# Kernel tuning notes

Measured on AMD Instinct MI355X. Metric: run time of the kernel, lower is better.

## Reference

```python
import jax, jax.numpy as jnp
import numpy as np

N = 50000
E = 600000
F_IN = 128
F_OUT = 128


def setup_inputs() -> dict:
    key = jax.random.key(0)
    k = jax.random.split(key, 8)
    x = jax.random.normal(k[0], (N, F_IN), dtype=jnp.float32)
    edge_index = jax.random.randint(k[1], (2, E), 0, N, dtype=jnp.int64)
    edge_weight = jax.random.uniform(k[2], (E,), dtype=jnp.float32)
    # glorot-initialized linear params (w1 is dead code in the original, kept for faithfulness)
    s = float(np.sqrt(6.0 / (F_IN + F_OUT)))
    W1 = jax.random.uniform(k[3], (F_IN, F_OUT), minval=-s, maxval=s, dtype=jnp.float32)
    b1 = jnp.zeros((F_OUT,), dtype=jnp.float32)
    W2 = jax.random.uniform(k[4], (F_IN, F_OUT), minval=-s, maxval=s, dtype=jnp.float32)
    b2 = jnp.zeros((F_OUT,), dtype=jnp.float32)
    a = jnp.full((1,), 0.5, dtype=jnp.float32)
    b = jnp.full((1,), 0.5, dtype=jnp.float32)
    return {"x": x, "edge_index": edge_index, "edge_weight": edge_weight,
            "W1": W1, "b1": b1, "W2": W2, "b2": b2, "a": a, "b": b}


def reference(x, edge_index, edge_weight, W1, b1, W2, b2, a, b):
    # wh_1 = self.w1(x)  (computed but unused in the original forward)
    wh_1 = x @ W1 + b1  # noqa: F841 (dead, DCE'd under jit)
    src, dst = edge_index[0], edge_index[1]
    # gather neighbor features [E, F_IN], scatter-sum to destination nodes [N, F_IN]
    x_j = jax.ops.segment_sum(x[src], dst, num_segments=N)
    wh_2 = x_j @ W2 + b2
    return wh_2
```

## Files before the change

kernel.cpp:

```cpp
#include <hip/hip_runtime.h>

#define F 128
#define CAP 64
#define TR 64
#define KC 32
#define LDA 36
#define LDW 160

__global__ __launch_bounds__(256) void init_kernel(
    const int* __restrict__ ei, const float* __restrict__ x,
    int* __restrict__ flag, int* __restrict__ zero_arr,
    unsigned int* __restrict__ xh, int N, int M)
{
    int i = blockIdx.x * 256 + threadIdx.x;
    if (i < M) {
        float2 v = reinterpret_cast<const float2*>(x)[i];
        unsigned ux = __float_as_uint(v.x);
        unsigned uy = __float_as_uint(v.y);
        unsigned lo = (ux + 0x7fffu + ((ux >> 16) & 1u)) >> 16;
        unsigned hi = (uy + 0x7fffu + ((uy >> 16) & 1u)) >> 16;
        xh[i] = lo | (hi << 16);
    }
    if (i < N) zero_arr[i] = 0;
    if (i == 0) {
        int or_hi = ei[1] | ei[3] | ei[5] | ei[7] | ei[9] | ei[11] | ei[13] | ei[15];
        *flag = (or_hi == 0) ? 1 : 0;
    }
}

__device__ __forceinline__ void load_edge(const int* __restrict__ ei, int is64,
                                          int E, int e, int& s, int& d)
{
    if (is64) {
        s = reinterpret_cast<const int2*>(ei)[e].x;
        d = reinterpret_cast<const int2*>(ei)[(size_t)E + e].x;
    } else {
        s = ei[e];
        d = ei[E + e];
    }
}

__global__ __launch_bounds__(256) void position_bucket_kernel(
    const int* __restrict__ ei, const int* __restrict__ flag_p,
    int* __restrict__ cursor, int* __restrict__ csr_src, int E)
{
    int e = blockIdx.x * 256 + threadIdx.x;
    if (e >= E) return;
    int s, d;
    load_edge(ei, *flag_p, E, e, s, d);
    int slot = atomicAdd(&cursor[d], 1);
    if (slot < CAP) csr_src[d * CAP + slot] = s;
}

__device__ __forceinline__ float4 bf16x4_to_f4(uint2 u)
{
    float4 f;
    f.x = __uint_as_float(u.x << 16);
    f.y = __uint_as_float(u.x & 0xffff0000u);
    f.z = __uint_as_float(u.y << 16);
    f.w = __uint_as_float(u.y & 0xffff0000u);
    return f;
}

__global__ __launch_bounds__(256) void gather_bucket_bf16_kernel(
    const unsigned int* __restrict__ xh, const int* __restrict__ ei,
    const int* __restrict__ flag_p, const int* __restrict__ cursor,
    const int* __restrict__ csr_src, float* __restrict__ agg, int N, int E)
{
    int node = blockIdx.x * 4 + (threadIdx.x >> 6);
    if (node >= N) return;
    int lane = threadIdx.x & 63;
    int half = lane >> 5;
    int col = lane & 31;
    int deg = cursor[node];

    const uint2* x2 = reinterpret_cast<const uint2*>(xh);
    float4 a0 = make_float4(0.f, 0.f, 0.f, 0.f);
    float4 a1 = make_float4(0.f, 0.f, 0.f, 0.f);

    if (deg <= CAP) {
        int sv = (lane < deg) ? csr_src[node * CAP + lane] : 0;
        int i = 0;
        for (; i + 3 < deg; i += 4) {
            int e0 = __shfl(sv, i + half);
            int e1 = __shfl(sv, i + 2 + half);
            float4 v0 = bf16x4_to_f4(x2[(size_t)e0 * 32 + col]);
            float4 v1 = bf16x4_to_f4(x2[(size_t)e1 * 32 + col]);
            a0.x += v0.x; a0.y += v0.y; a0.z += v0.z; a0.w += v0.w;
            a1.x += v1.x; a1.y += v1.y; a1.z += v1.z; a1.w += v1.w;
        }
        for (; i + 1 < deg; i += 2) {
            int e0 = __shfl(sv, i + half);
            float4 v0 = bf16x4_to_f4(x2[(size_t)e0 * 32 + col]);
            a0.x += v0.x; a0.y += v0.y; a0.z += v0.z; a0.w += v0.w;
        }
        if (i < deg) {
            int e0 = __shfl(sv, i);
            if (half == 0) {
                float4 v = bf16x4_to_f4(x2[(size_t)e0 * 32 + col]);
                a0.x += v.x; a0.y += v.y; a0.z += v.z; a0.w += v.w;
            }
        }
    } else {
        int is64 = *flag_p;
        for (int base = 0; base < E; base += 64) {
            int e = base + lane;
            int s = 0, d = -1;
            if (e < E) load_edge(ei, is64, E, e, s, d);
            unsigned long long m = __ballot(d == node);
            while (m) {
                int i = __ffsll((long long)m) - 1;
                m &= m - 1;
                int sb = __shfl(s, i);
                float4 v = bf16x4_to_f4(x2[(size_t)sb * 32 + col]);
                if (half == 0) { a0.x += v.x; a0.y += v.y; a0.z += v.z; a0.w += v.w; }
            }
        }
    }
    a0.x += a1.x; a0.y += a1.y; a0.z += a1.z; a0.w += a1.w;
    a0.x += __shfl_xor(a0.x, 32);
    a0.y += __shfl_xor(a0.y, 32);
    a0.z += __shfl_xor(a0.z, 32);
    a0.w += __shfl_xor(a0.w, 32);
    if (half == 0)
        reinterpret_cast<float4*>(agg)[(size_t)node * 32 + col] = a0;
}

__global__ __launch_bounds__(256) void hist_kernel(
    const int* __restrict__ ei, const int* __restrict__ flag_p,
    int* __restrict__ counts, int E)
{
    int e = blockIdx.x * 256 + threadIdx.x;
    if (e >= E) return;
    int s, d;
    load_edge(ei, *flag_p, E, e, s, d);
    atomicAdd(&counts[d], 1);
}

__global__ __launch_bounds__(256) void scan1_kernel(
    const int* __restrict__ counts, int* __restrict__ locoff,
    int* __restrict__ cursor, int* __restrict__ blocksums, int N)
{
    __shared__ int sh[256];
    int t = threadIdx.x;
    int i = blockIdx.x * 256 + t;
    int v = (i < N) ? counts[i] : 0;
    sh[t] = v;
    __syncthreads();
    int inc = v;
    #pragma unroll
    for (int ofs = 1; ofs < 256; ofs <<= 1) {
        int add = (t >= ofs) ? sh[t - ofs] : 0;
        __syncthreads();
        inc += add;
        sh[t] = inc;
        __syncthreads();
    }
    if (i < N) { locoff[i] = inc - v; cursor[i] = inc - v; }
    if (t == 255) blocksums[blockIdx.x] = inc;
}

__global__ __launch_bounds__(256) void scan2_kernel(
    int* __restrict__ blocksums, int* __restrict__ blockoffs, int nblk)
{
    __shared__ int sh[256];
    int t = threadIdx.x;
    int v = (t < nblk) ? blocksums[t] : 0;
    sh[t] = v;
    __syncthreads();
    int inc = v;
    #pragma unroll
    for (int ofs = 1; ofs < 256; ofs <<= 1) {
        int add = (t >= ofs) ? sh[t - ofs] : 0;
        __syncthreads();
        inc += add;
        sh[t] = inc;
        __syncthreads();
    }
    if (t < nblk) blockoffs[t] = inc - v;
}

__global__ __launch_bounds__(256) void position_kernel(
    const int* __restrict__ ei, const int* __restrict__ flag_p,
    int* __restrict__ cursor, const int* __restrict__ blockoffs,
    int* __restrict__ csr_src, int E)
{
    int e = blockIdx.x * 256 + threadIdx.x;
    if (e >= E) return;
    int s, d;
    load_edge(ei, *flag_p, E, e, s, d);
    int pos = atomicAdd(&cursor[d], 1) + blockoffs[d >> 8];
    csr_src[pos] = s;
}

__global__ __launch_bounds__(256) void gather_csr_bf16_kernel(
    const unsigned int* __restrict__ xh, const int* __restrict__ locoff,
    const int* __restrict__ blockoffs, const int* __restrict__ counts,
    const int* __restrict__ csr_src, float* __restrict__ agg, int N)
{
    int node = blockIdx.x * 4 + (threadIdx.x >> 6);
    if (node >= N) return;
    int lane = threadIdx.x & 63;
    int half = lane >> 5;
    int col = lane & 31;
    int start = locoff[node] + blockoffs[node >> 8];
    int deg = counts[node];

    const uint2* x2 = reinterpret_cast<const uint2*>(xh);
    float4 a0 = make_float4(0.f, 0.f, 0.f, 0.f);
    float4 a1 = make_float4(0.f, 0.f, 0.f, 0.f);

    for (int base = 0; base < deg; base += 64) {
        int rem = deg - base; if (rem > 64) rem = 64;
        int sv = (lane < rem) ? csr_src[start + base + lane] : 0;
        int i = 0;
        for (; i + 3 < rem; i += 4) {
            int e0 = __shfl(sv, i + half);
            int e1 = __shfl(sv, i + 2 + half);
            float4 v0 = bf16x4_to_f4(x2[(size_t)e0 * 32 + col]);
            float4 v1 = bf16x4_to_f4(x2[(size_t)e1 * 32 + col]);
            a0.x += v0.x; a0.y += v0.y; a0.z += v0.z; a0.w += v0.w;
            a1.x += v1.x; a1.y += v1.y; a1.z += v1.z; a1.w += v1.w;
        }
        for (; i + 1 < rem; i += 2) {
            int e0 = __shfl(sv, i + half);
            float4 v0 = bf16x4_to_f4(x2[(size_t)e0 * 32 + col]);
            a0.x += v0.x; a0.y += v0.y; a0.z += v0.z; a0.w += v0.w;
        }
        if (i < rem) {
            int e0 = __shfl(sv, i);
            if (half == 0) {
                float4 v = bf16x4_to_f4(x2[(size_t)e0 * 32 + col]);
                a0.x += v.x; a0.y += v.y; a0.z += v.z; a0.w += v.w;
            }
        }
    }
    a0.x += a1.x; a0.y += a1.y; a0.z += a1.z; a0.w += a1.w;
    a0.x += __shfl_xor(a0.x, 32);
    a0.y += __shfl_xor(a0.y, 32);
    a0.z += __shfl_xor(a0.z, 32);
    a0.w += __shfl_xor(a0.w, 32);
    if (half == 0)
        reinterpret_cast<float4*>(agg)[(size_t)node * 32 + col] = a0;
}

__global__ __launch_bounds__(256) void gather_csr_f32_kernel(
    const float* __restrict__ x, const int* __restrict__ locoff,
    const int* __restrict__ blockoffs, const int* __restrict__ counts,
    const int* __restrict__ csr_src, float* __restrict__ agg, int N)
{
    int node = blockIdx.x * 4 + (threadIdx.x >> 6);
    if (node >= N) return;
    int lane = threadIdx.x & 63;
    int half = lane >> 5;
    int col = lane & 31;
    int start = locoff[node] + blockoffs[node >> 8];
    int deg = counts[node];

    const float4* x4 = reinterpret_cast<const float4*>(x);
    float4 a0 = make_float4(0.f, 0.f, 0.f, 0.f);
    float4 a1 = make_float4(0.f, 0.f, 0.f, 0.f);

    for (int base = 0; base < deg; base += 64) {
        int rem = deg - base; if (rem > 64) rem = 64;
        int sv = (lane < rem) ? csr_src[start + base + lane] : 0;
        int i = 0;
        for (; i + 3 < rem; i += 4) {
            int e0 = __shfl(sv, i + half);
            int e1 = __shfl(sv, i + 2 + half);
            float4 v0 = x4[(size_t)e0 * 32 + col];
            float4 v1 = x4[(size_t)e1 * 32 + col];
            a0.x += v0.x; a0.y += v0.y; a0.z += v0.z; a0.w += v0.w;
            a1.x += v1.x; a1.y += v1.y; a1.z += v1.z; a1.w += v1.w;
        }
        for (; i + 1 < rem; i += 2) {
            int e0 = __shfl(sv, i + half);
            float4 v0 = x4[(size_t)e0 * 32 + col];
            a0.x += v0.x; a0.y += v0.y; a0.z += v0.z; a0.w += v0.w;
        }
        if (i < rem) {
            int e0 = __shfl(sv, i);
            if (half == 0) {
                float4 v = x4[(size_t)e0 * 32 + col];
                a0.x += v.x; a0.y += v.y; a0.z += v.z; a0.w += v.w;
            }
        }
    }
    a0.x += a1.x; a0.y += a1.y; a0.z += a1.z; a0.w += a1.w;
    a0.x += __shfl_xor(a0.x, 32);
    a0.y += __shfl_xor(a0.y, 32);
    a0.z += __shfl_xor(a0.z, 32);
    a0.w += __shfl_xor(a0.w, 32);
    if (half == 0)
        reinterpret_cast<float4*>(agg)[(size_t)node * 32 + col] = a0;
}

__global__ __launch_bounds__(256) void scatter_kernel(
    const float* __restrict__ x, const int* __restrict__ ei,
    const int* __restrict__ flag_p, float* __restrict__ agg, int E)
{
    int tid = blockIdx.x * 256 + threadIdx.x;
    int e = tid >> 5;
    if (e >= E) return;
    int c = (tid & 31) << 2;
    int s, d;
    load_edge(ei, *flag_p, E, e, s, d);
    float4 v = *reinterpret_cast<const float4*>(x + (size_t)s * F + c);
    float* o = agg + (size_t)d * F + c;
    unsafeAtomicAdd(o + 0, v.x);
    unsafeAtomicAdd(o + 1, v.y);
    unsafeAtomicAdd(o + 2, v.z);
    unsafeAtomicAdd(o + 3, v.w);
}

__global__ __launch_bounds__(256) void gemm_kernel(
    float* __restrict__ io, const float* __restrict__ W,
    const float* __restrict__ bias, int N)
{
    __shared__ float sA[TR * LDA];
    __shared__ float sW[KC * LDW];
    const int t = threadIdx.x;
    const int row0 = blockIdx.x * TR;
    const int g = t & 7;
    const int r = t >> 3;

    float acc[2][16];
    #pragma unroll
    for (int i = 0; i < 2; ++i)
        #pragma unroll
        for (int j = 0; j < 16; ++j) acc[i][j] = 0.0f;

    for (int kc = 0; kc < F; kc += KC) {
        #pragma unroll
        for (int u = 0; u < 2; ++u) {
            int idx = u * 256 + t;
            int row = idx >> 3;
            int k4 = (idx & 7) * 4;
            int grow = row0 + row;
            float4 v = (grow < N)
                ? *reinterpret_cast<const float4*>(io + (size_t)grow * F + kc + k4)
                : make_float4(0.f, 0.f, 0.f, 0.f);
            *reinterpret_cast<float4*>(&sA[row * LDA + k4]) = v;
        }
        #pragma unroll
        for (int u = 0; u < 4; ++u) {
            int idx = u * 256 + t;
            int kk = idx >> 5;
            int f4 = (idx & 31) * 4;
            float4 v = *reinterpret_cast<const float4*>(W + (size_t)(kc + kk) * F + f4);
            int chunk = f4 >> 4;
            int within = f4 & 15;
            *reinterpret_cast<float4*>(&sW[kk * LDW + chunk * 20 + within]) = v;
        }
        __syncthreads();

        #pragma unroll 8
        for (int kk = 0; kk < KC; ++kk) {
            const float* wp = &sW[kk * LDW + g * 20];
            const float4 w0 = *reinterpret_cast<const float4*>(wp + 0);
            const float4 w1 = *reinterpret_cast<const float4*>(wp + 4);
            const float4 w2 = *reinterpret_cast<const float4*>(wp + 8);
            const float4 w3 = *reinterpret_cast<const float4*>(wp + 12);
            #pragma unroll
            for (int i = 0; i < 2; ++i) {
                const float xv = sA[(r * 2 + i) * LDA + kk];
                acc[i][0]  += xv * w0.x;  acc[i][1]  += xv * w0.y;
                acc[i][2]  += xv * w0.z;  acc[i][3]  += xv * w0.w;
                acc[i][4]  += xv * w1.x;  acc[i][5]  += xv * w1.y;
                acc[i][6]  += xv * w1.z;  acc[i][7]  += xv * w1.w;
                acc[i][8]  += xv * w2.x;  acc[i][9]  += xv * w2.y;
                acc[i][10] += xv * w2.z;  acc[i][11] += xv * w2.w;
                acc[i][12] += xv * w3.x;  acc[i][13] += xv * w3.y;
                acc[i][14] += xv * w3.z;  acc[i][15] += xv * w3.w;
            }
        }
        __syncthreads();
    }

    float bv[16];
    #pragma unroll
    for (int j = 0; j < 16; ++j) bv[j] = bias[g * 16 + j];
    #pragma unroll
    for (int i = 0; i < 2; ++i) {
        int row = row0 + r * 2 + i;
        if (row < N) {
            float* o = io + (size_t)row * F + g * 16;
            #pragma unroll
            for (int j4 = 0; j4 < 4; ++j4) {
                float4 v;
                v.x = acc[i][j4 * 4 + 0] + bv[j4 * 4 + 0];
                v.y = acc[i][j4 * 4 + 1] + bv[j4 * 4 + 1];
                v.z = acc[i][j4 * 4 + 2] + bv[j4 * 4 + 2];
                v.w = acc[i][j4 * 4 + 3] + bv[j4 * 4 + 3];
                *reinterpret_cast<float4*>(o + j4 * 4) = v;
            }
        }
    }
}

extern "C" void kernel_launch(void* const* d_in, const int* in_sizes, int n_in,
                              void* d_out, int out_size, void* d_ws, size_t ws_size,
                              hipStream_t stream) {
    const float* x  = (const float*)d_in[0];
    const int*   ei = (const int*)d_in[1];
    const float* W2 = (const float*)d_in[5];
    const float* b2 = (const float*)d_in[6];
    float* out = (float*)d_out;

    const int N = in_sizes[0] / F;
    const int E = in_sizes[2];
    const int nblk = (N + 255) / 256;
    const int M = N * (F / 2);
    const int eblk = (E + 255) / 256;

    int* ws = (int*)d_ws;
    size_t needA = (size_t)(16 + N + N * CAP + M) * sizeof(int);
    size_t needC = (size_t)(16 + 3 * N + 2 * nblk + E) * sizeof(int);
    size_t needB = needC + (size_t)M * sizeof(int);

    if (ws_size >= needA) {
        int* flag    = ws;
        int* cursor  = flag + 16;
        int* csr_src = cursor + N;
        unsigned int* xh = (unsigned int*)(csr_src + (size_t)N * CAP);

        int iblk = ((M > N ? M : N) + 255) / 256;
        init_kernel<<<iblk, 256, 0, stream>>>(ei, x, flag, cursor, xh, N, M);
        position_bucket_kernel<<<eblk, 256, 0, stream>>>(ei, flag, cursor, csr_src, E);
        gather_bucket_bf16_kernel<<<(N + 3) / 4, 256, 0, stream>>>(
            xh, ei, flag, cursor, csr_src, out, N, E);
    } else if (ws_size >= needC) {
        int* flag      = ws;
        int* counts    = flag + 16;
        int* locoff    = counts + N;
        int* cursor    = locoff + N;
        int* blocksums = cursor + N;
        int* blockoffs = blocksums + nblk;
        int* csr_src   = blockoffs + nblk;
        unsigned int* xh = (unsigned int*)(csr_src + E);
        int do_bf16 = (ws_size >= needB) ? 1 : 0;
        int Mx = do_bf16 ? M : 0;

        int iblk = (((Mx > N ? Mx : N)) + 255) / 256;
        init_kernel<<<iblk, 256, 0, stream>>>(ei, x, flag, counts, xh, N, Mx);
        hist_kernel<<<eblk, 256, 0, stream>>>(ei, flag, counts, E);
        scan1_kernel<<<nblk, 256, 0, stream>>>(counts, locoff, cursor, blocksums, N);
        scan2_kernel<<<1, 256, 0, stream>>>(blocksums, blockoffs, nblk);
        position_kernel<<<eblk, 256, 0, stream>>>(ei, flag, cursor, blockoffs, csr_src, E);
        if (do_bf16)
            gather_csr_bf16_kernel<<<(N + 3) / 4, 256, 0, stream>>>(
                xh, locoff, blockoffs, counts, csr_src, out, N);
        else
            gather_csr_f32_kernel<<<(N + 3) / 4, 256, 0, stream>>>(
                x, locoff, blockoffs, counts, csr_src, out, N);
    } else {
        int* flag = ws;
        init_kernel<<<1, 64, 0, stream>>>(ei, x, flag, flag + 16, nullptr, 0, 0);
        hipMemsetAsync(out, 0, (size_t)N * F * sizeof(float), stream);
        scatter_kernel<<<(E * 32 + 255) / 256, 256, 0, stream>>>(x, ei, flag, out, E);
    }

    gemm_kernel<<<(N + TR - 1) / TR, 256, 0, stream>>>(out, W2, b2, N);
}
```

Baseline: 187.3 us.

## Fuse gather with GEMM and merge bf16 conversion into edge bucketing

The main path now fuses neighbour aggregation with the dense W2 projection. Each block gathers 64 rows into shared memory and multiplies them by W2 directly, so the aggregated matrix is no longer written to and re-read from global memory. The bf16 conversion of x is folded into the edge positioning kernel, which also loads two edges per thread with vector loads. A small zero kernel replaces the old init. The risk is lower gather parallelism, since each wave handles 16 rows in sequence and fewer blocks are launched. The large shared-memory footprint of about 54 KB may also limit occupancy.

```diff
diff --git a/kernel.cpp b/kernel.cpp
--- a/kernel.cpp
+++ b/kernel.cpp
@@ -2,10 +2,230 @@
 
 #define F 128
 #define CAP 64
+#define KC 32
+#define LDAF 132
+#define LDW 160
 #define TR 64
-#define KC 32
 #define LDA 36
-#define LDW 160
+
+__global__ __launch_bounds__(256) void zero_kernel(
+    const int* __restrict__ ei, int* __restrict__ flag,
+    int* __restrict__ cursor, int N)
+{
+    int i = blockIdx.x * 256 + threadIdx.x;
+    if (i < N) cursor[i] = 0;
+    if (i == 0) {
+        int or_hi = ei[1] | ei[3] | ei[5] | ei[7] | ei[9] | ei[11] | ei[13] | ei[15];
+        *flag = (or_hi == 0) ? 1 : 0;
+    }
+}
+
+__device__ __forceinline__ void load_edge(const int* __restrict__ ei, int is64,
+                                          int E, int e, int& s, int& d)
+{
+    if (is64) {
+        s = reinterpret_cast<const int2*>(ei)[e].x;
+        d = reinterpret_cast<const int2*>(ei)[(size_t)E + e].x;
+    } else {
+        s = ei[e];
+        d = ei[E + e];
+    }
+}
+
+__global__ __launch_bounds__(256) void posconv_kernel(
+    const int* __restrict__ ei, const float* __restrict__ x,
+    const int* __restrict__ flag_p, int* __restrict__ cursor,
+    int* __restrict__ csr_src, unsigned int* __restrict__ xh,
+    int E, int M)
+{
+    const int tid = blockIdx.x * 256 + threadIdx.x;
+    const int T = gridDim.x * 256;
+    const int is64 = *flag_p;
+
+    int e0 = 2 * tid;
+    if (e0 < E) {
+        if (e0 + 1 < E) {
+            int s0, d0, s1, d1;
+            if (is64) {
+                int4 sv = reinterpret_cast<const int4*>(ei)[tid];
+                int4 dv = reinterpret_cast<const int4*>(ei)[(size_t)(E >> 1) + tid];
+                s0 = sv.x; s1 = sv.z; d0 = dv.x; d1 = dv.z;
+            } else {
+                int2 sv = reinterpret_cast<const int2*>(ei)[tid];
+                int2 dv = reinterpret_cast<const int2*>(ei)[(size_t)(E >> 1) + tid];
+                s0 = sv.x; s1 = sv.y; d0 = dv.x; d1 = dv.y;
+            }
+            int slot0 = atomicAdd(&cursor[d0], 1);
+            int slot1 = atomicAdd(&cursor[d1], 1);
+            if (slot0 < CAP) csr_src[d0 * CAP + slot0] = s0;
+            if (slot1 < CAP) csr_src[d1 * CAP + slot1] = s1;
+        } else {
+            int s, d;
+            load_edge(ei, is64, E, e0, s, d);
+            int slot = atomicAdd(&cursor[d], 1);
+            if (slot < CAP) csr_src[d * CAP + slot] = s;
+        }
+    }
+
+    const float2* x2 = reinterpret_cast<const float2*>(x);
+    for (int j = tid; j < M; j += T) {
+        float2 v = x2[j];
+        unsigned ux = __float_as_uint(v.x);
+        unsigned uy = __float_as_uint(v.y);
+        unsigned lo = (ux + 0x7fffu + ((ux >> 16) & 1u)) >> 16;
+        unsigned hi = (uy + 0x7fffu + ((uy >> 16) & 1u)) >> 16;
+        xh[j] = lo | (hi << 16);
+    }
+}
+
+__device__ __forceinline__ float4 bf16x4_to_f4(uint2 u)
+{
+    float4 f;
+    f.x = __uint_as_float(u.x << 16);
+    f.y = __uint_as_float(u.x & 0xffff0000u);
+    f.z = __uint_as_float(u.y << 16);
+    f.w = __uint_as_float(u.y & 0xffff0000u);
+    return f;
+}
+
+__global__ __launch_bounds__(256) void gather_gemm_kernel(
+    const unsigned int* __restrict__ xh, const int* __restrict__ ei,
+    const int* __restrict__ flag_p, const int* __restrict__ cursor,
+    const int* __restrict__ csr_src, const float* __restrict__ W,
+    const float* __restrict__ bias, float* __restrict__ out, int N, int E)
+{
+    __shared__ float sA[64 * LDAF];
+    __shared__ float sW[KC * LDW];
+    const int t = threadIdx.x;
+    const int row0 = blockIdx.x * 64;
+    const int w = t >> 6;
+    const int lane = t & 63;
+    const int half = lane >> 5;
+    const int col = lane & 31;
+
+    const uint2* x2 = reinterpret_cast<const uint2*>(xh);
+
+    for (int j = 0; j < 16; ++j) {
+        int lrow = w * 16 + j;
+        int node = row0 + lrow;
+        float4 a0 = make_float4(0.f, 0.f, 0.f, 0.f);
+        float4 a1 = make_float4(0.f, 0.f, 0.f, 0.f);
+        if (node < N) {
+            int deg = cursor[node];
+            if (deg <= CAP) {
+                int sv = (lane < deg) ? csr_src[node * CAP + lane] : 0;
+                int i = 0;
+                for (; i + 3 < deg; i += 4) {
+                    int e0 = __shfl(sv, i + half);
+                    int e1 = __shfl(sv, i + 2 + half);
+                    float4 v0 = bf16x4_to_f4(x2[(size_t)e0 * 32 + col]);
+                    float4 v1 = bf16x4_to_f4(x2[(size_t)e1 * 32 + col]);
+                    a0.x += v0.x; a0.y += v0.y; a0.z += v0.z; a0.w += v0.w;
+                    a1.x += v1.x; a1.y += v1.y; a1.z += v1.z; a1.w += v1.w;
+                }
+                for (; i + 1 < deg; i += 2) {
+                    int e0 = __shfl(sv, i + half);
+                    float4 v0 = bf16x4_to_f4(x2[(size_t)e0 * 32 + col]);
+                    a0.x += v0.x; a0.y += v0.y; a0.z += v0.z; a0.w += v0.w;
+                }
+                if (i < deg) {
+                    int e0 = __shfl(sv, i);
+                    if (half == 0) {
+                        float4 v = bf16x4_to_f4(x2[(size_t)e0 * 32 + col]);
+                        a0.x += v.x; a0.y += v.y; a0.z += v.z; a0.w += v.w;
+                    }
+                }
+            } else {
+                int is64 = *flag_p;
+                for (int base = 0; base < E; base += 64) {
+                    int e = base + lane;
+                    int s = 0, d = -1;
+                    if (e < E) load_edge(ei, is64, E, e, s, d);
+                    unsigned long long m = __ballot(d == node);
+                    while (m) {
+                        int i = __ffsll((long long)m) - 1;
+                        m &= m - 1;
+                        int sb = __shfl(s, i);
+                        float4 v = bf16x4_to_f4(x2[(size_t)sb * 32 + col]);
+                        if (half == 0) { a0.x += v.x; a0.y += v.y; a0.z += v.z; a0.w += v.w; }
+                    }
+                }
+            }
+        }
+        a0.x += a1.x; a0.y += a1.y; a0.z += a1.z; a0.w += a1.w;
+        a0.x += __shfl_xor(a0.x, 32);
+        a0.y += __shfl_xor(a0.y, 32);
+        a0.z += __shfl_xor(a0.z, 32);
+        a0.w += __shfl_xor(a0.w, 32);
+        if (half == 0)
+            *reinterpret_cast<float4*>(&sA[lrow * LDAF + col * 4]) = a0;
+    }
+    __syncthreads();
+
+    const int g = t & 7;
+    const int r = t >> 3;
+    float acc[2][16];
+    #pragma unroll
+    for (int i = 0; i < 2; ++i)
+        #pragma unroll
+        for (int j = 0; j < 16; ++j) acc[i][j] = 0.0f;
+
+    for (int kc = 0; kc < F; kc += KC) {
+        #pragma unroll
+        for (int u = 0; u < 4; ++u) {
+            int idx = u * 256 + t;
+            int kk = idx >> 5;
+            int f4 = (idx & 31) * 4;
+            float4 v = *reinterpret_cast<const float4*>(W + (size_t)(kc + kk) * F + f4);
+            int chunk = f4 >> 4;
+            int within = f4 & 15;
+            *reinterpret_cast<float4*>(&sW[kk * LDW + chunk * 20 + within]) = v;
+        }
+        __syncthreads();
+
+        #pragma unroll 8
+        for (int kk = 0; kk < KC; ++kk) {
+            const float* wp = &sW[kk * LDW + g * 20];
+            const float4 w0 = *reinterpret_cast<const float4*>(wp + 0);
+            const float4 w1 = *reinterpret_cast<const float4*>(wp + 4);
+            const float4 w2 = *reinterpret_cast<const float4*>(wp + 8);
+            const float4 w3 = *reinterpret_cast<const float4*>(wp + 12);
+            #pragma unroll
+            for (int i = 0; i < 2; ++i) {
+                const float xv = sA[(r * 2 + i) * LDAF + kc + kk];
+                acc[i][0]  += xv * w0.x;  acc[i][1]  += xv * w0.y;
+                acc[i][2]  += xv * w0.z;  acc[i][3]  += xv * w0.w;
+                acc[i][4]  += xv * w1.x;  acc[i][5]  += xv * w1.y;
+                acc[i][6]  += xv * w1.z;  acc[i][7]  += xv * w1.w;
+                acc[i][8]  += xv * w2.x;  acc[i][9]  += xv * w2.y;
+                acc[i][10] += xv * w2.z;  acc[i][11] += xv * w2.w;
+                acc[i][12] += xv * w3.x;  acc[i][13] += xv * w3.y;
+                acc[i][14] += xv * w3.z;  acc[i][15] += xv * w3.w;
+            }
+        }
+        __syncthreads();
+    }
+
+    float bv[16];
+    #pragma unroll
+    for (int j = 0; j < 16; ++j) bv[j] = bias[g * 16 + j];
+    #pragma unroll
+    for (int i = 0; i < 2; ++i) {
+        int row = row0 + r * 2 + i;
+        if (row < N) {
+            float* o = out + (size_t)row * F + g * 16;
+            #pragma unroll
+            for (int j4 = 0; j4 < 4; ++j4) {
+                float4 v;
+                v.x = acc[i][j4 * 4 + 0] + bv[j4 * 4 + 0];
+                v.y = acc[i][j4 * 4 + 1] + bv[j4 * 4 + 1];
+                v.z = acc[i][j4 * 4 + 2] + bv[j4 * 4 + 2];
+                v.w = acc[i][j4 * 4 + 3] + bv[j4 * 4 + 3];
+                *reinterpret_cast<float4*>(o + j4 * 4) = v;
+            }
+        }
+    }
+}
 
 __global__ __launch_bounds__(256) void init_kernel(
     const int* __restrict__ ei, const float* __restrict__ x,
@@ -28,18 +248,6 @@
     }
 }
 
-__device__ __forceinline__ void load_edge(const int* __restrict__ ei, int is64,
-                                          int E, int e, int& s, int& d)
-{
-    if (is64) {
-        s = reinterpret_cast<const int2*>(ei)[e].x;
-        d = reinterpret_cast<const int2*>(ei)[(size_t)E + e].x;
-    } else {
-        s = ei[e];
-        d = ei[E + e];
-    }
-}
-
 __global__ __launch_bounds__(256) void position_bucket_kernel(
     const int* __restrict__ ei, const int* __restrict__ flag_p,
     int* __restrict__ cursor, int* __restrict__ csr_src, int E)
@@ -52,18 +260,8 @@
     if (slot < CAP) csr_src[d * CAP + slot] = s;
 }
 
-__device__ __forceinline__ float4 bf16x4_to_f4(uint2 u)
-{
-    float4 f;
-    f.x = __uint_as_float(u.x << 16);
-    f.y = __uint_as_float(u.x & 0xffff0000u);
-    f.z = __uint_as_float(u.y << 16);
-    f.w = __uint_as_float(u.y & 0xffff0000u);
-    return f;
-}
-
-__global__ __launch_bounds__(256) void gather_bucket_bf16_kernel(
-    const unsigned int* __restrict__ xh, const int* __restrict__ ei,
+__global__ __launch_bounds__(256) void gather_bucket_f32_kernel(
+    const float* __restrict__ x, const int* __restrict__ ei,
     const int* __restrict__ flag_p, const int* __restrict__ cursor,
     const int* __restrict__ csr_src, float* __restrict__ agg, int N, int E)
 {
@@ -74,7 +272,7 @@
     int col = lane & 31;
     int deg = cursor[node];
 
-    const uint2* x2 = reinterpret_cast<const uint2*>(xh);
+    const float4* x4 = reinterpret_cast<const float4*>(x);
     float4 a0 = make_float4(0.f, 0.f, 0.f, 0.f);
     float4 a1 = make_float4(0.f, 0.f, 0.f, 0.f);
 
@@ -84,20 +282,20 @@
         for (; i + 3 < deg; i += 4) {
             int e0 = __shfl(sv, i + half);
             int e1 = __shfl(sv, i + 2 + half);
-            float4 v0 = bf16x4_to_f4(x2[(size_t)e0 * 32 + col]);
-            float4 v1 = bf16x4_to_f4(x2[(size_t)e1 * 32 + col]);
+            float4 v0 = x4[(size_t)e0 * 32 + col];
+            float4 v1 = x4[(size_t)e1 * 32 + col];
             a0.x += v0.x; a0.y += v0.y; a0.z += v0.z; a0.w += v0.w;
             a1.x += v1.x; a1.y += v1.y; a1.z += v1.z; a1.w += v1.w;
         }
         for (; i + 1 < deg; i += 2) {
             int e0 = __shfl(sv, i + half);
-            float4 v0 = bf16x4_to_f4(x2[(size_t)e0 * 32 + col]);
+            float4 v0 = x4[(size_t)e0 * 32 + col];
             a0.x += v0.x; a0.y += v0.y; a0.z += v0.z; a0.w += v0.w;
         }
         if (i < deg) {
             int e0 = __shfl(sv, i);
             if (half == 0) {
-                float4 v = bf16x4_to_f4(x2[(size_t)e0 * 32 + col]);
+                float4 v = x4[(size_t)e0 * 32 + col];
                 a0.x += v.x; a0.y += v.y; a0.z += v.z; a0.w += v.w;
             }
         }
@@ -112,177 +310,8 @@
                 int i = __ffsll((long long)m) - 1;
                 m &= m - 1;
                 int sb = __shfl(s, i);
-                float4 v = bf16x4_to_f4(x2[(size_t)sb * 32 + col]);
+                float4 v = x4[(size_t)sb * 32 + col];
                 if (half == 0) { a0.x += v.x; a0.y += v.y; a0.z += v.z; a0.w += v.w; }
-            }
-        }
-    }
-    a0.x += a1.x; a0.y += a1.y; a0.z += a1.z; a0.w += a1.w;
-    a0.x += __shfl_xor(a0.x, 32);
-    a0.y += __shfl_xor(a0.y, 32);
-    a0.z += __shfl_xor(a0.z, 32);
-    a0.w += __shfl_xor(a0.w, 32);
-    if (half == 0)
-        reinterpret_cast<float4*>(agg)[(size_t)node * 32 + col] = a0;
-}
-
-__global__ __launch_bounds__(256) void hist_kernel(
-    const int* __restrict__ ei, const int* __restrict__ flag_p,
-    int* __restrict__ counts, int E)
-{
-    int e = blockIdx.x * 256 + threadIdx.x;
-    if (e >= E) return;
-    int s, d;
-    load_edge(ei, *flag_p, E, e, s, d);
-    atomicAdd(&counts[d], 1);
-}
-
-__global__ __launch_bounds__(256) void scan1_kernel(
-    const int* __restrict__ counts, int* __restrict__ locoff,
-    int* __restrict__ cursor, int* __restrict__ blocksums, int N)
-{
-    __shared__ int sh[256];
-    int t = threadIdx.x;
-    int i = blockIdx.x * 256 + t;
-    int v = (i < N) ? counts[i] : 0;
-    sh[t] = v;
-    __syncthreads();
-    int inc = v;
-    #pragma unroll
-    for (int ofs = 1; ofs < 256; ofs <<= 1) {
-        int add = (t >= ofs) ? sh[t - ofs] : 0;
-        __syncthreads();
-        inc += add;
-        sh[t] = inc;
-        __syncthreads();
-    }
-    if (i < N) { locoff[i] = inc - v; cursor[i] = inc - v; }
-    if (t == 255) blocksums[blockIdx.x] = inc;
-}
-
-__global__ __launch_bounds__(256) void scan2_kernel(
-    int* __restrict__ blocksums, int* __restrict__ blockoffs, int nblk)
-{
-    __shared__ int sh[256];
-    int t = threadIdx.x;
-    int v = (t < nblk) ? blocksums[t] : 0;
-    sh[t] = v;
-    __syncthreads();
-    int inc = v;
-    #pragma unroll
-    for (int ofs = 1; ofs < 256; ofs <<= 1) {
-        int add = (t >= ofs) ? sh[t - ofs] : 0;
-        __syncthreads();
-        inc += add;
-        sh[t] = inc;
-        __syncthreads();
-    }
-    if (t < nblk) blockoffs[t] = inc - v;
-}
-
-__global__ __launch_bounds__(256) void position_kernel(
-    const int* __restrict__ ei, const int* __restrict__ flag_p,
-    int* __restrict__ cursor, const int* __restrict__ blockoffs,
-    int* __restrict__ csr_src, int E)
-{
-    int e = blockIdx.x * 256 + threadIdx.x;
-    if (e >= E) return;
-    int s, d;
-    load_edge(ei, *flag_p, E, e, s, d);
-    int pos = atomicAdd(&cursor[d], 1) + blockoffs[d >> 8];
-    csr_src[pos] = s;
-}
-
-__global__ __launch_bounds__(256) void gather_csr_bf16_kernel(
-    const unsigned int* __restrict__ xh, const int* __restrict__ locoff,
-    const int* __restrict__ blockoffs, const int* __restrict__ counts,
-    const int* __restrict__ csr_src, float* __restrict__ agg, int N)
-{
-    int node = blockIdx.x * 4 + (threadIdx.x >> 6);
-    if (node >= N) return;
-    int lane = threadIdx.x & 63;
-    int half = lane >> 5;
-    int col = lane & 31;
-    int start = locoff[node] + blockoffs[node >> 8];
-    int deg = counts[node];
-
-    const uint2* x2 = reinterpret_cast<const uint2*>(xh);
-    float4 a0 = make_float4(0.f, 0.f, 0.f, 0.f);
-    float4 a1 = make_float4(0.f, 0.f, 0.f, 0.f);
-
-    for (int base = 0; base < deg; base += 64) {
-        int rem = deg - base; if (rem > 64) rem = 64;
-        int sv = (lane < rem) ? csr_src[start + base + lane] : 0;
-        int i = 0;
-        for (; i + 3 < rem; i += 4) {
-            int e0 = __shfl(sv, i + half);
-            int e1 = __shfl(sv, i + 2 + half);
-            float4 v0 = bf16x4_to_f4(x2[(size_t)e0 * 32 + col]);
-            float4 v1 = bf16x4_to_f4(x2[(size_t)e1 * 32 + col]);
-            a0.x += v0.x; a0.y += v0.y; a0.z += v0.z; a0.w += v0.w;
-            a1.x += v1.x; a1.y += v1.y; a1.z += v1.z; a1.w += v1.w;
-        }
-        for (; i + 1 < rem; i += 2) {
-            int e0 = __shfl(sv, i + half);
-            float4 v0 = bf16x4_to_f4(x2[(size_t)e0 * 32 + col]);
-            a0.x += v0.x; a0.y += v0.y; a0.z += v0.z; a0.w += v0.w;
-        }
-        if (i < rem) {
-            int e0 = __shfl(sv, i);
-            if (half == 0) {
-                float4 v = bf16x4_to_f4(x2[(size_t)e0 * 32 + col]);
-                a0.x += v.x; a0.y += v.y; a0.z += v.z; a0.w += v.w;
-            }
-        }
-    }
-    a0.x += a1.x; a0.y += a1.y; a0.z += a1.z; a0.w += a1.w;
-    a0.x += __shfl_xor(a0.x, 32);
-    a0.y += __shfl_xor(a0.y, 32);
-    a0.z += __shfl_xor(a0.z, 32);
-    a0.w += __shfl_xor(a0.w, 32);
-    if (half == 0)
-        reinterpret_cast<float4*>(agg)[(size_t)node * 32 + col] = a0;
-}
-
-__global__ __launch_bounds__(256) void gather_csr_f32_kernel(
-    const float* __restrict__ x, const int* __restrict__ locoff,
-    const int* __restrict__ blockoffs, const int* __restrict__ counts,
-    const int* __restrict__ csr_src, float* __restrict__ agg, int N)
-{
-    int node = blockIdx.x * 4 + (threadIdx.x >> 6);
-    if (node >= N) return;
-    int lane = threadIdx.x & 63;
-    int half = lane >> 5;
-    int col = lane & 31;
-    int start = locoff[node] + blockoffs[node >> 8];
-    int deg = counts[node];
-
-    const float4* x4 = reinterpret_cast<const float4*>(x);
-    float4 a0 = make_float4(0.f, 0.f, 0.f, 0.f);
-    float4 a1 = make_float4(0.f, 0.f, 0.f, 0.f);
-
-    for (int base = 0; base < deg; base += 64) {
-        int rem = deg - base; if (rem > 64) rem = 64;
-        int sv = (lane < rem) ? csr_src[start + base + lane] : 0;
-        int i = 0;
-        for (; i + 3 < rem; i += 4) {
-            int e0 = __shfl(sv, i + half);
-            int e1 = __shfl(sv, i + 2 + half);
-            float4 v0 = x4[(size_t)e0 * 32 + col];
-            float4 v1 = x4[(size_t)e1 * 32 + col];
-            a0.x += v0.x; a0.y += v0.y; a0.z += v0.z; a0.w += v0.w;
-            a1.x += v1.x; a1.y += v1.y; a1.z += v1.z; a1.w += v1.w;
-        }
-        for (; i + 1 < rem; i += 2) {
-            int e0 = __shfl(sv, i + half);
-            float4 v0 = x4[(size_t)e0 * 32 + col];
-            a0.x += v0.x; a0.y += v0.y; a0.z += v0.z; a0.w += v0.w;
-        }
-        if (i < rem) {
-            int e0 = __shfl(sv, i);
-            if (half == 0) {
-                float4 v = x4[(size_t)e0 * 32 + col];
-                a0.x += v.x; a0.y += v.y; a0.z += v.z; a0.w += v.w;
             }
         }
     }
@@ -414,9 +443,8 @@
     const int eblk = (E + 255) / 256;
 
     int* ws = (int*)d_ws;
-    size_t needA = (size_t)(16 + N + N * CAP + M) * sizeof(int);
-    size_t needC = (size_t)(16 + 3 * N + 2 * nblk + E) * sizeof(int);
-    size_t needB = needC + (size_t)M * sizeof(int);
+    size_t needA = (size_t)(16 + N + (size_t)N * CAP + M) * sizeof(int);
+    size_t needB = (size_t)(16 + N + (size_t)N * CAP) * sizeof(int);
 
     if (ws_size >= needA) {
         int* flag    = ws;
@@ -424,41 +452,25 @@
         int* csr_src = cursor + N;
         unsigned int* xh = (unsigned int*)(csr_src + (size_t)N * CAP);
 
-        int iblk = ((M > N ? M : N) + 255) / 256;
-        init_kernel<<<iblk, 256, 0, stream>>>(ei, x, flag, cursor, xh, N, M);
+        zero_kernel<<<nblk, 256, 0, stream>>>(ei, flag, cursor, N);
+        int pblk = ((E + 1) / 2 + 255) / 256;
+        posconv_kernel<<<pblk, 256, 0, stream>>>(ei, x, flag, cursor, csr_src, xh, E, M);
+        gather_gemm_kernel<<<(N + 63) / 64, 256, 0, stream>>>(
+            xh, ei, flag, cursor, csr_src, W2, b2, out, N, E);
+    } else if (ws_size >= needB) {
+        int* flag    = ws;
+        int* cursor  = flag + 16;
+        int* csr_src = cursor + N;
+        init_kernel<<<nblk, 256, 0, stream>>>(ei, x, flag, cursor, nullptr, N, 0);
         position_bucket_kernel<<<eblk, 256, 0, stream>>>(ei, flag, cursor, csr_src, E);
-        gather_bucket_bf16_kernel<<<(N + 3) / 4, 256, 0, stream>>>(
-            xh, ei, flag, cursor, csr_src, out, N, E);
-    } else if (ws_size >= needC) {
-        int* flag      = ws;
-        int* counts    = flag + 16;
-        int* locoff    = counts + N;
-        int* cursor    = locoff + N;
-        int* blocksums = cursor + N;
-        int* blockoffs = blocksums + nblk;
-        int* csr_src   = blockoffs + nblk;
-        unsigned int* xh = (unsigned int*)(csr_src + E);
-        int do_bf16 = (ws_size >= needB) ? 1 : 0;
-        int Mx = do_bf16 ? M : 0;
-
-        int iblk = (((Mx > N ? Mx : N)) + 255) / 256;
-        init_kernel<<<iblk, 256, 0, stream>>>(ei, x, flag, counts, xh, N, Mx);
-        hist_kernel<<<eblk, 256, 0, stream>>>(ei, flag, counts, E);
-        scan1_kernel<<<nblk, 256, 0, stream>>>(counts, locoff, cursor, blocksums, N);
-        scan2_kernel<<<1, 256, 0, stream>>>(blocksums, blockoffs, nblk);
-        position_kernel<<<eblk, 256, 0, stream>>>(ei, flag, cursor, blockoffs, csr_src, E);
-        if (do_bf16)
-            gather_csr_bf16_kernel<<<(N + 3) / 4, 256, 0, stream>>>(
-                xh, locoff, blockoffs, counts, csr_src, out, N);
-        else
-            gather_csr_f32_kernel<<<(N + 3) / 4, 256, 0, stream>>>(
-                x, locoff, blockoffs, counts, csr_src, out, N);
+        gather_bucket_f32_kernel<<<(N + 3) / 4, 256, 0, stream>>>(
+            x, ei, flag, cursor, csr_src, out, N, E);
+        gemm_kernel<<<(N + TR - 1) / TR, 256, 0, stream>>>(out, W2, b2, N);
     } else {
         int* flag = ws;
         init_kernel<<<1, 64, 0, stream>>>(ei, x, flag, flag + 16, nullptr, 0, 0);
         hipMemsetAsync(out, 0, (size_t)N * F * sizeof(float), stream);
         scatter_kernel<<<(E * 32 + 255) / 256, 256, 0, stream>>>(x, ei, flag, out, E);
-    }
-
-    gemm_kernel<<<(N + TR - 1) / TR, 256, 0, stream>>>(out, W2, b2, N);
-}
+        gemm_kernel<<<(N + TR - 1) / TR, 256, 0, stream>>>(out, W2, b2, N);
+    }
+}
```

Result: slower. 244.7 us (+30.6%).
